# Performance work log

Hardware: AMD Instinct MI355X
Metric: run time of the kernel (lower is better)

The kernel has to match this reference:

```python
import jax, jax.numpy as jnp
import numpy as np

jax.config.update("jax_enable_x64", True)  # gaus_fit runs in float64, matching torch .double()

STAB_NB = 1e-15


def _gaus_fit(x):
    """Weighted Gaussian regression. x: (bn, x_len, col_len), values > 0."""
    col_len = x.shape[-1]
    col = jnp.arange(col_len, dtype=jnp.float64)          # (col_len,)
    y = x.astype(jnp.float64)
    y2 = y * y
    lny = jnp.log(y)
    y2l = y2 * lny
    x1, x2, x3, x4 = col, col**2, col**3, col**4
    s_y2    = jnp.sum(y2, -1)
    s_xy2   = jnp.sum(x1 * y2, -1)
    s_x2y2  = jnp.sum(x2 * y2, -1)
    s_x3y2  = jnp.sum(x3 * y2, -1)
    s_x4y2  = jnp.sum(x4 * y2, -1)
    s_y2l   = jnp.sum(y2l, -1)
    s_xy2l  = jnp.sum(x1 * y2l, -1)
    s_x2y2l = jnp.sum(x2 * y2l, -1)
    b_num = (s_x2y2**2 * s_xy2l - s_y2 * s_x4y2 * s_xy2l + s_xy2 * s_x4y2 * s_y2l
             + s_y2 * s_x3y2 * s_x2y2l - s_x2y2 * s_x3y2 * s_y2l - s_xy2 * s_x2y2 * s_x2y2l)
    c_num = (s_x2y2l * s_xy2**2 - s_xy2l * s_xy2 * s_x2y2 - s_x3y2 * s_y2l * s_xy2
             + s_y2l * s_x2y2**2 - s_y2 * s_x2y2l * s_x2y2 + s_y2 * s_x3y2 * s_xy2l)
    # clamp |c_num| away from zero (sign(0)*STAB -> 0, same as torch.sign)
    c_num = jnp.where(jnp.abs(c_num) < STAB_NB, jnp.sign(c_num) * STAB_NB, c_num)
    mu = -b_num / (2.0 * c_num)
    c_din = (s_x4y2 * s_xy2**2 - 2.0 * s_xy2 * s_x2y2 * s_x3y2 + s_x2y2**3
             - s_y2 * s_x4y2 * s_x2y2 + s_y2 * s_x3y2**2)
    sigma = -0.5 * c_din / c_num
    sigma = jnp.where(sigma < 1.0, 1.0, sigma)
    return mu.astype(jnp.float32), sigma.astype(jnp.float32)


def _newton_sol(g_mean, g_sigma, w_comp):
    """Solve (H_pair + diag(1/sigma)) x = mean/sigma via dense inverse (faithful to source)."""
    n = g_mean.shape[1]
    w = w_comp.astype(jnp.float32)[0]
    main = jnp.concatenate([2.0 * w[None], 4.0 * w * jnp.ones(n - 2, jnp.float32), 2.0 * w[None]])
    off = -2.0 * w * jnp.ones(n - 1, jnp.float32)
    hess_pair = jnp.diag(main) + jnp.diag(off, 1) + jnp.diag(off, -1)   # (n, n)
    sig_rev = 1.0 / g_sigma                                              # (bn, n)
    hess = hess_pair[None, :, :] + jnp.eye(n, dtype=jnp.float32) * sig_rev[:, :, None]
    hess_inv = jnp.linalg.inv(hess)                                      # (bn, n, n)
    p = g_mean * sig_rev
    return jnp.einsum('bij,bj->bi', hess_inv, p)


def setup_inputs() -> dict:
    key = jax.random.key(0)
    k1, _ = jax.random.split(key)
    x = jax.random.normal(k1, (32, 1024, 512), dtype=jnp.float32)  # (BN, X_LEN, COL_LEN) logits
    w_comp = jnp.ones((1,), jnp.float32) * 1e-05                   # learned CRF weight
    return {"x": x, "w_comp": w_comp}


def reference(x, w_comp):
    # softmax over column (depth) axis
    p = jax.nn.softmax(x, axis=-1)
    # normalize_prob: min-max to [0,1] then +0.001
    pmin = jnp.min(p, -1, keepdims=True)
    pmax = jnp.max(p, -1, keepdims=True)
    pn = (p - pmin) / (pmax - pmin) + 0.001
    mu, sigma = _gaus_fit(pn)
    return _newton_sol(mu, sigma, w_comp)  # (BN, X_LEN), tr_flag=True path
```

## Files before the change

kernel.cpp:

```cpp
#include <hip/hip_runtime.h>
#include <hip/hip_bf16.h>
#include <math.h>

#define BN 32
#define XLEN 1024
#define COLS 512
#define ROWS (BN * XLEN)
#define STAB 1e-15

typedef float v2f __attribute__((ext_vector_type(2)));

#define HW_EXP2(x) __builtin_amdgcn_exp2f(x)
#define HW_LOG2(x) __builtin_amdgcn_logf(x)

__global__ __launch_bounds__(256, 8) void gaus_fit_kernel(
    const float* __restrict__ x, float* __restrict__ mu_out,
    float* __restrict__ sig_out) {
  const int lane = threadIdx.x & 63;
  const int wid  = threadIdx.x >> 6;
  const int sub  = lane & 15;
  const int row  = blockIdx.x * 16 + wid * 4 + (lane >> 4);

  const v2f* rp2 = (const v2f*)(x + (size_t)row * COLS);
  v2f ve[16];
#pragma unroll
  for (int j = 0; j < 8; ++j) {
    ve[2 * j]     = rp2[32 * j + 2 * sub];
    ve[2 * j + 1] = rp2[32 * j + 2 * sub + 1];
  }

  v2f mx2 = ve[0], xn2 = ve[0];
#pragma unroll
  for (int k = 1; k < 16; ++k) {
    mx2 = __builtin_elementwise_max(mx2, ve[k]);
    xn2 = __builtin_elementwise_min(xn2, ve[k]);
  }
  float mx = fmaxf(mx2.x, mx2.y);
  float xn = fminf(xn2.x, xn2.y);
#pragma unroll
  for (int m = 8; m >= 1; m >>= 1) {
    mx = fmaxf(mx, __shfl_xor(mx, m, 64));
    xn = fminf(xn, __shfl_xor(xn, m, 64));
  }

  const float LOG2E = 1.44269504089f;
  const float mxs = mx * LOG2E;
  const v2f L2E2 = {LOG2E, LOG2E};
  const v2f NMXS = {-mxs, -mxs};
  v2f S2a = {0.0f, 0.0f}, S2b = {0.0f, 0.0f};
#pragma unroll
  for (int k = 0; k < 16; k += 2) {
    const v2f xs0 = __builtin_elementwise_fma(ve[k], L2E2, NMXS);
    const v2f xs1 = __builtin_elementwise_fma(ve[k + 1], L2E2, NMXS);
    ve[k].x     = HW_EXP2(xs0.x);
    ve[k].y     = HW_EXP2(xs0.y);
    ve[k + 1].x = HW_EXP2(xs1.x);
    ve[k + 1].y = HW_EXP2(xs1.y);
    S2a += ve[k];
    S2b += ve[k + 1];
  }
  const v2f S2 = S2a + S2b;
  float S = S2.x + S2.y;
#pragma unroll
  for (int m = 8; m >= 1; m >>= 1) S += __shfl_xor(S, m, 64);

  const float invS   = 1.0f / S;
  const float emin   = HW_EXP2(fmaf(xn, LOG2E, -mxs));
  const float pmin   = emin * invS;
  const float pmax   = invS;
  const float invden = 1.0f / (pmax - pmin);
  const float CA     = invS * invden;
  const float CB     = fmaf(-pmin, invden, 0.001f);
  const v2f CA2 = {CA, CA}, CB2 = {CB, CB};

  const float bb = (float)(4 * sub) * (1.0f / 512.0f);
  v2f u0 = {0, 0}, u1 = {0, 0}, u2 = {0, 0}, u3 = {0, 0}, u4 = {0, 0};
  v2f w0 = {0, 0}, w1 = {0, 0}, w2 = {0, 0};

#define GF_PAIR(j, h)                                                         \
  {                                                                           \
    const int   k   = 2 * (j) + (h);                                          \
    const float off = (float)(64 * (j) + 2 * (h)) * (1.0f / 512.0f);          \
    const v2f xh = {bb + off, bb + off + 0.001953125f};                       \
    const v2f pn = __builtin_elementwise_fma(ve[k], CA2, CB2);                \
    v2f l2;                                                                   \
    l2.x = HW_LOG2(pn.x);                                                     \
    l2.y = HW_LOG2(pn.y);                                                     \
    const v2f y2  = pn * pn;                                                  \
    const v2f y2l = y2 * l2;                                                  \
    const v2f x2  = xh * xh;                                                  \
    const v2f x3  = x2 * xh;                                                  \
    const v2f x4  = x2 * x2;                                                  \
    u0 += y2;                                                                 \
    u1 = __builtin_elementwise_fma(xh, y2, u1);                               \
    u2 = __builtin_elementwise_fma(x2, y2, u2);                               \
    u3 = __builtin_elementwise_fma(x3, y2, u3);                               \
    u4 = __builtin_elementwise_fma(x4, y2, u4);                               \
    w0 += y2l;                                                                \
    w1 = __builtin_elementwise_fma(xh, y2l, w1);                              \
    w2 = __builtin_elementwise_fma(x2, y2l, w2);                              \
  }

#pragma unroll
  for (int j = 0; j < 8; ++j) {
    GF_PAIR(j, 0)
    GF_PAIR(j, 1)
  }
#undef GF_PAIR

  double d0 = (double)u0.x + (double)u0.y;
  double d1 = (double)u1.x + (double)u1.y;
  double d2 = (double)u2.x + (double)u2.y;
  double d3 = (double)u3.x + (double)u3.y;
  double d4 = (double)u4.x + (double)u4.y;
  double e0 = (double)w0.x + (double)w0.y;
  double e1 = (double)w1.x + (double)w1.y;
  double e2 = (double)w2.x + (double)w2.y;
#pragma unroll
  for (int m = 8; m >= 1; m >>= 1) {
    d0 += __shfl_xor(d0, m, 64);
    d1 += __shfl_xor(d1, m, 64);
    d2 += __shfl_xor(d2, m, 64);
    d3 += __shfl_xor(d3, m, 64);
    d4 += __shfl_xor(d4, m, 64);
    e0 += __shfl_xor(e0, m, 64);
    e1 += __shfl_xor(e1, m, 64);
    e2 += __shfl_xor(e2, m, 64);
  }

  if (sub == 0) {
    const double LN2D = 0.6931471805599453;
    const double s_y2    = d0;
    const double s_xy2   = d1 * 512.0;
    const double s_x2y2  = d2 * 262144.0;
    const double s_x3y2  = d3 * 134217728.0;
    const double s_x4y2  = d4 * 68719476736.0;
    const double s_y2l   = e0 * LN2D;
    const double s_xy2l  = (e1 * 512.0) * LN2D;
    const double s_x2y2l = (e2 * 262144.0) * LN2D;
    const double A2 = s_x2y2 * s_x2y2;
    double b_num = A2 * s_xy2l - s_y2 * s_x4y2 * s_xy2l
                 + s_xy2 * s_x4y2 * s_y2l + s_y2 * s_x3y2 * s_x2y2l
                 - s_x2y2 * s_x3y2 * s_y2l - s_xy2 * s_x2y2 * s_x2y2l;
    double c_num = s_x2y2l * s_xy2 * s_xy2 - s_xy2l * s_xy2 * s_x2y2
                 - s_x3y2 * s_y2l * s_xy2 + s_y2l * A2
                 - s_y2 * s_x2y2l * s_x2y2 + s_y2 * s_x3y2 * s_xy2l;
    if (fabs(c_num) < STAB) {
      c_num = (c_num > 0.0) ? STAB : ((c_num < 0.0) ? -STAB : 0.0);
    }
    const double mu = -b_num / (2.0 * c_num);
    const double c_din = s_x4y2 * s_xy2 * s_xy2
                       - 2.0 * s_xy2 * s_x2y2 * s_x3y2 + s_x2y2 * A2
                       - s_y2 * s_x4y2 * s_x2y2 + s_y2 * s_x3y2 * s_x3y2;
    double sigma = -0.5 * c_din / c_num;
    if (sigma < 1.0) sigma = 1.0;
    mu_out[row]  = (float)mu;
    sig_out[row] = (float)sigma;
  }
}

__global__ __launch_bounds__(1024) void pcr_solve_kernel(
    const float* __restrict__ mu, const float* __restrict__ sigma,
    const float* __restrict__ w_comp, float* __restrict__ out) {
  __shared__ float A[2][XLEN], B[2][XLEN], C[2][XLEN], D[2][XLEN], R[2][XLEN];
  const int i = threadIdx.x;
  const int g = blockIdx.x * XLEN + i;

  const float w = w_comp[0];
  const float offf  = -2.0f * w;
  const float mainw = (i == 0 || i == XLEN - 1) ? (2.0f * w) : (4.0f * w);
  const float sr = 1.0f / sigma[g];
  const float bf = mainw + sr;
  const float df = mu[g] * sr;

  A[0][i] = (i == 0) ? 0.0f : offf;
  C[0][i] = (i == XLEN - 1) ? 0.0f : offf;
  B[0][i] = bf;
  D[0][i] = df;
  R[0][i] = 1.0f / bf;
  __syncthreads();

  int cur = 0;
  for (int s = 1; s < XLEN; s <<= 1) {
    const float ai = A[cur][i], bi = B[cur][i], ci = C[cur][i], di = D[cur][i];
    float am = 0.0f, cm = 0.0f, dm = 0.0f, rm = 0.0f;
    float ap = 0.0f, cp = 0.0f, dp = 0.0f, rp = 0.0f;
    if (i >= s) {
      am = A[cur][i - s]; cm = C[cur][i - s]; dm = D[cur][i - s]; rm = R[cur][i - s];
    }
    if (i + s < XLEN) {
      ap = A[cur][i + s]; cp = C[cur][i + s]; dp = D[cur][i + s]; rp = R[cur][i + s];
    }
    const float k1 = ai * rm;
    const float k2 = ci * rp;
    const float nb = bi - k1 * cm - k2 * ap;
    const float nd = di - k1 * dm - k2 * dp;
    const int nxt = cur ^ 1;
    A[nxt][i] = -k1 * am;
    C[nxt][i] = -k2 * cp;
    B[nxt][i] = nb;
    D[nxt][i] = nd;
    R[nxt][i] = 1.0f / nb;
    __syncthreads();
    cur = nxt;
  }

  out[g] = D[cur][i] * R[cur][i];
}

extern "C" void kernel_launch(void* const* d_in, const int* in_sizes, int n_in,
                              void* d_out, int out_size, void* d_ws, size_t ws_size,
                              hipStream_t stream) {
  const float* x      = (const float*)d_in[0];
  const float* w_comp = (const float*)d_in[1];
  float* out = (float*)d_out;

  float* mu_ws  = (float*)d_ws;
  float* sig_ws = mu_ws + ROWS;

  gaus_fit_kernel<<<ROWS / 16, 256, 0, stream>>>(x, mu_ws, sig_ws);
  pcr_solve_kernel<<<BN, XLEN, 0, stream>>>(mu_ws, sig_ws, w_comp, out);
}
```

Measured before the change: 25.91 us.

## Fuse gaus fit and tridiagonal PCR solve via last-block-per-batch atomic counter

Merges the two kernels into one. Each block atomically increments a per-batch counter, and the last of the 64 blocks for a batch runs the PCR tridiagonal solve with 256 threads covering 4 rows each. This removes the second kernel launch and its dependency gap. In exchange it adds a memset launch, atomics and fences, and runs the serial PCR on fewer threads with extra reciprocal work, which could lengthen the tail of the kernel.

```diff
diff --git a/kernel.cpp b/kernel.cpp
--- a/kernel.cpp
+++ b/kernel.cpp
@@ -12,10 +12,15 @@
 
 #define HW_EXP2(x) __builtin_amdgcn_exp2f(x)
 #define HW_LOG2(x) __builtin_amdgcn_logf(x)
-
-__global__ __launch_bounds__(256, 8) void gaus_fit_kernel(
-    const float* __restrict__ x, float* __restrict__ mu_out,
-    float* __restrict__ sig_out) {
+#define HW_RCP(x)  __builtin_amdgcn_rcpf(x)
+
+__global__ __launch_bounds__(256, 8) void fused_kernel(
+    const float* __restrict__ x, const float* __restrict__ w_comp,
+    float* __restrict__ mu_ws, float* __restrict__ sig_ws,
+    unsigned* __restrict__ cnt, float* __restrict__ out) {
+  __shared__ float As[XLEN], Bs[XLEN], Cs[XLEN], Ds[XLEN];
+  __shared__ int go;
+
   const int lane = threadIdx.x & 63;
   const int wid  = threadIdx.x >> 6;
   const int sub  = lane & 15;
@@ -154,58 +159,71 @@
                        - s_y2 * s_x4y2 * s_x2y2 + s_y2 * s_x3y2 * s_x3y2;
     double sigma = -0.5 * c_din / c_num;
     if (sigma < 1.0) sigma = 1.0;
-    mu_out[row]  = (float)mu;
-    sig_out[row] = (float)sigma;
-  }
-}
-
-__global__ __launch_bounds__(1024) void pcr_solve_kernel(
-    const float* __restrict__ mu, const float* __restrict__ sigma,
-    const float* __restrict__ w_comp, float* __restrict__ out) {
-  __shared__ float A[2][XLEN], B[2][XLEN], C[2][XLEN], D[2][XLEN], R[2][XLEN];
-  const int i = threadIdx.x;
-  const int g = blockIdx.x * XLEN + i;
-
+    mu_ws[row]  = (float)mu;
+    sig_ws[row] = (float)sigma;
+  }
+
+  const int batch = blockIdx.x >> 6;
+  __syncthreads();
+  if (threadIdx.x == 0) {
+    __threadfence();
+    go = (atomicAdd(&cnt[batch], 1u) == 63u) ? 1 : 0;
+  }
+  __syncthreads();
+  if (!go) return;
+  __threadfence();
+
+  const int base = batch * XLEN;
   const float w = w_comp[0];
-  const float offf  = -2.0f * w;
-  const float mainw = (i == 0 || i == XLEN - 1) ? (2.0f * w) : (4.0f * w);
-  const float sr = 1.0f / sigma[g];
-  const float bf = mainw + sr;
-  const float df = mu[g] * sr;
-
-  A[0][i] = (i == 0) ? 0.0f : offf;
-  C[0][i] = (i == XLEN - 1) ? 0.0f : offf;
-  B[0][i] = bf;
-  D[0][i] = df;
-  R[0][i] = 1.0f / bf;
+  const float offf = -2.0f * w;
+  const int t = threadIdx.x;
+#pragma unroll
+  for (int q = 0; q < 4; ++q) {
+    const int i = t + 256 * q;
+    const float sr = 1.0f / sig_ws[base + i];
+    const float mainw = (i == 0 || i == XLEN - 1) ? (2.0f * w) : (4.0f * w);
+    As[i] = (i == 0) ? 0.0f : offf;
+    Cs[i] = (i == XLEN - 1) ? 0.0f : offf;
+    Bs[i] = mainw + sr;
+    Ds[i] = mu_ws[base + i] * sr;
+  }
   __syncthreads();
 
-  int cur = 0;
   for (int s = 1; s < XLEN; s <<= 1) {
-    const float ai = A[cur][i], bi = B[cur][i], ci = C[cur][i], di = D[cur][i];
-    float am = 0.0f, cm = 0.0f, dm = 0.0f, rm = 0.0f;
-    float ap = 0.0f, cp = 0.0f, dp = 0.0f, rp = 0.0f;
-    if (i >= s) {
-      am = A[cur][i - s]; cm = C[cur][i - s]; dm = D[cur][i - s]; rm = R[cur][i - s];
+    float na[4], nb[4], nc[4], nd[4];
+#pragma unroll
+    for (int q = 0; q < 4; ++q) {
+      const int i = t + 256 * q;
+      const float ai = As[i], bi = Bs[i], ci = Cs[i], di = Ds[i];
+      float am = 0.0f, cm = 0.0f, dm = 0.0f, rm = 0.0f;
+      float ap = 0.0f, cp = 0.0f, dp = 0.0f, rp = 0.0f;
+      if (i >= s) {
+        am = As[i - s]; cm = Cs[i - s]; dm = Ds[i - s]; rm = HW_RCP(Bs[i - s]);
+      }
+      if (i + s < XLEN) {
+        ap = As[i + s]; cp = Cs[i + s]; dp = Ds[i + s]; rp = HW_RCP(Bs[i + s]);
+      }
+      const float k1 = ai * rm;
+      const float k2 = ci * rp;
+      nb[q] = bi - k1 * cm - k2 * ap;
+      nd[q] = di - k1 * dm - k2 * dp;
+      na[q] = -k1 * am;
+      nc[q] = -k2 * cp;
     }
-    if (i + s < XLEN) {
-      ap = A[cur][i + s]; cp = C[cur][i + s]; dp = D[cur][i + s]; rp = R[cur][i + s];
+    __syncthreads();
+#pragma unroll
+    for (int q = 0; q < 4; ++q) {
+      const int i = t + 256 * q;
+      As[i] = na[q]; Bs[i] = nb[q]; Cs[i] = nc[q]; Ds[i] = nd[q];
     }
-    const float k1 = ai * rm;
-    const float k2 = ci * rp;
-    const float nb = bi - k1 * cm - k2 * ap;
-    const float nd = di - k1 * dm - k2 * dp;
-    const int nxt = cur ^ 1;
-    A[nxt][i] = -k1 * am;
-    C[nxt][i] = -k2 * cp;
-    B[nxt][i] = nb;
-    D[nxt][i] = nd;
-    R[nxt][i] = 1.0f / nb;
     __syncthreads();
-    cur = nxt;
-  }
-
-  out[g] = D[cur][i] * R[cur][i];
+  }
+
+#pragma unroll
+  for (int q = 0; q < 4; ++q) {
+    const int i = t + 256 * q;
+    out[base + i] = Ds[i] / Bs[i];
+  }
 }
 
 extern "C" void kernel_launch(void* const* d_in, const int* in_sizes, int n_in,
@@ -217,7 +235,8 @@
 
   float* mu_ws  = (float*)d_ws;
   float* sig_ws = mu_ws + ROWS;
-
-  gaus_fit_kernel<<<ROWS / 16, 256, 0, stream>>>(x, mu_ws, sig_ws);
-  pcr_solve_kernel<<<BN, XLEN, 0, stream>>>(mu_ws, sig_ws, w_comp, out);
+  unsigned* cnt = (unsigned*)(sig_ws + ROWS);
+
+  hipMemsetAsync((void*)cnt, 0, BN * sizeof(unsigned), stream);
+  fused_kernel<<<ROWS / 16, 256, 0, stream>>>(x, w_comp, mu_ws, sig_ws, cnt, out);
 }
```

After: 97.57 us. 277% more time.
